# Kernel optimization log

Measured on AMD Instinct MI355X. Metric: run time of the kernel, lower is better.

Reference implementation:

```python
import jax, jax.numpy as jnp
import numpy as np
import math

B, S, D, H = 4, 2048, 1024, 16
HD = D // H  # 64


def setup_inputs() -> dict:
    key = jax.random.key(0)
    ks = jax.random.split(key, 12)
    s_in = 1.0 / math.sqrt(D)
    inp = {
        "x_v": jax.random.normal(ks[0], (B, S, D), jnp.float32),
        "x_k": jax.random.normal(ks[1], (B, S, D), jnp.float32),
        "x_q": jax.random.normal(ks[2], (B, S, D), jnp.float32),
        "mask": jax.random.randint(ks[3], (B, S, S), 0, 2, jnp.int32),
        "Wq": jax.random.normal(ks[4], (H, D, HD), jnp.float32) * s_in,
        "bq": jax.random.normal(ks[5], (H, HD), jnp.float32) * s_in,
        "Wk": jax.random.normal(ks[6], (H, D, HD), jnp.float32) * s_in,
        "bk": jax.random.normal(ks[7], (H, HD), jnp.float32) * s_in,
        "Wv": jax.random.normal(ks[8], (H, D, HD), jnp.float32) * s_in,
        "bv": jax.random.normal(ks[9], (H, HD), jnp.float32) * s_in,
        "Wo": jax.random.normal(ks[10], (D, D), jnp.float32) * s_in,
        "bo": jax.random.normal(ks[11], (D,), jnp.float32) * s_in,
    }
    return inp


def reference(x_v, x_k, x_q, mask, Wq, bq, Wk, bk, Wv, bv, Wo, bo):
    # Batched per-head projections: [B,S,D] x [H,D,E] -> [B,H,S,E]
    q = jnp.einsum("bsd,hde->bhse", x_q, Wq) + bq[None, :, None, :]
    k = jnp.einsum("bsd,hde->bhse", x_k, Wk) + bk[None, :, None, :]
    v = jnp.einsum("bsd,hde->bhse", x_v, Wv) + bv[None, :, None, :]
    scale = 1.0 / math.sqrt(HD)
    scores = jnp.einsum("bhqe,bhke->bhqk", q, k) * scale  # [B,H,Sq,Sk]
    # Faithful to original: masked positions are set to 0 (not -inf) BEFORE softmax
    scores = jnp.where(mask[:, None, :, :] == 0, 0.0, scores)
    attn = jax.nn.softmax(scores, axis=-1)
    z = jnp.einsum("bhqk,bhke->bhqe", attn, v)  # [B,H,Sq,E]
    # Concat over heads in head order (matches torch.cat along dim=2)
    z = z.transpose(0, 2, 1, 3).reshape(B, S, D)
    return z @ Wo + bo
```

## Files before the change

### kernel.cpp

```cpp
#include <hip/hip_runtime.h>

typedef unsigned short u16;
typedef unsigned long long u64;
typedef __attribute__((ext_vector_type(8))) short bf16x8;
typedef __attribute__((ext_vector_type(4))) float f32x4;

#define LD 72
#define C_SCALE 0.18033688011112043f

__device__ __forceinline__ u16 f2b(float x) {
  union { float f; unsigned u; } c; c.f = x;
  unsigned r = (c.u + 0x7fffu + ((c.u >> 16) & 1u)) >> 16;
  return (u16)r;
}

__device__ __forceinline__ unsigned pk2(float a, float b) {
#if __has_builtin(__builtin_amdgcn_cvt_pk_bf16_f32)
  typedef __attribute__((ext_vector_type(2))) __bf16 b2;
  b2 r = __builtin_amdgcn_cvt_pk_bf16_f32(a, b);
  union { b2 v; unsigned u; } c; c.v = r;
  return c.u;
#else
  union { float f; unsigned u; } x, y;
  x.f = a; y.f = b;
  return ((x.u + 0x8000u) >> 16) | ((y.u + 0x8000u) & 0xffff0000u);
#endif
}

__device__ __forceinline__ float blo(int w) {
  union { int i; float f; } c; c.i = w << 16; return c.f;
}
__device__ __forceinline__ float bhi(int w) {
  union { int i; float f; } c; c.i = w & 0xffff0000; return c.f;
}

__device__ __forceinline__ void gll16(const u16* g, u16* l) {
  __builtin_amdgcn_global_load_lds(
      (const __attribute__((address_space(1))) void*)g,
      (__attribute__((address_space(3))) void*)l, 16, 0, 0);
}

__global__ __launch_bounds__(256) void cvt_bf16_3(
    const float4* __restrict__ s0, const float4* __restrict__ s1,
    const float4* __restrict__ s2, ushort4* __restrict__ d0,
    ushort4* __restrict__ d1, ushort4* __restrict__ d2, int n4) {
  const int z = blockIdx.y;
  const float4* src = z == 0 ? s0 : z == 1 ? s1 : s2;
  ushort4* dst = z == 0 ? d0 : z == 1 ? d1 : d2;
  int stride = gridDim.x * 256;
  for (int i = blockIdx.x * 256 + threadIdx.x; i < n4; i += stride) {
    float4 v = src[i];
    ushort4 o = { f2b(v.x), f2b(v.y), f2b(v.z), f2b(v.w) };
    dst[i] = o;
  }
}

__global__ __launch_bounds__(256) void transpose_cvt_all(
    const float* __restrict__ Wq, const float* __restrict__ Wk,
    const float* __restrict__ Wv, const float* __restrict__ Wo,
    u16* __restrict__ wq_t, u16* __restrict__ wk_t,
    u16* __restrict__ wv_t, u16* __restrict__ wo_t) {
  __shared__ u16 tile[64][65];
  const int id = blockIdx.x;
  const int which = id >> 8, sub = id & 255;
  const float* s;
  u16* d;
  int R, C, r0, c0;
  if (which < 3) {
    const float* W = which == 0 ? Wq : which == 1 ? Wk : Wv;
    u16* D = which == 0 ? wq_t : which == 1 ? wk_t : wv_t;
    int h = sub >> 4, rt = sub & 15;
    s = W + (size_t)h * 1024 * 64;
    d = D + (size_t)h * 64 * 1024;
    R = 1024; C = 64; r0 = rt * 64; c0 = 0;
  } else {
    s = Wo; d = wo_t;
    R = 1024; C = 1024; r0 = ((sub >> 4) & 15) * 64; c0 = (sub & 15) * 64;
  }
  const int t = threadIdx.x;
#pragma unroll
  for (int rep = 0; rep < 16; ++rep) {
    int idx = rep * 256 + t;
    int i = idx >> 6, j = idx & 63;
    tile[j][i] = f2b(s[(size_t)(r0 + i) * C + c0 + j]);
  }
  __syncthreads();
#pragma unroll
  for (int rep = 0; rep < 16; ++rep) {
    int idx = rep * 256 + t;
    int jj = idx >> 6, ii = idx & 63;
    d[(size_t)(c0 + jj) * R + r0 + ii] = tile[jj][ii];
  }
}

__global__ __launch_bounds__(256) void expand_mask(
    const int4* __restrict__ m, ushort4* __restrict__ mb, int n4) {
  int stride = gridDim.x * 256;
  for (int i = blockIdx.x * 256 + threadIdx.x; i < n4; i += stride) {
    int4 v = m[i];
    ushort4 o = { (u16)(v.x ? 0x3f80 : 0), (u16)(v.y ? 0x3f80 : 0),
                  (u16)(v.z ? 0x3f80 : 0), (u16)(v.w ? 0x3f80 : 0) };
    mb[i] = o;
  }
}

__device__ __forceinline__ void gemm_core(
    const u16* __restrict__ A, const u16* __restrict__ W,
    u16* Asm, u16* Bsm, int s0, int n0, int wv, int lane,
    int m16, int q4, f32x4 acc[4][4]) {
  const int rsub = lane >> 3, csub = lane & 7;
  const int wr = (wv & 1) * 64, wc = (wv >> 1) * 64;
  for (int k0 = 0; k0 < 1024; k0 += 64) {
    __syncthreads();
#pragma unroll
    for (int i = 0; i < 4; ++i) {
      int chunk = wv * 4 + i;
      gll16(A + (size_t)(s0 + chunk * 8 + rsub) * 1024 + k0 + csub * 8,
            Asm + chunk * 512 + lane * 8);
      gll16(W + (size_t)(n0 + chunk * 8 + rsub) * 1024 + k0 + csub * 8,
            Bsm + chunk * 512 + lane * 8);
    }
    __syncthreads();
#pragma unroll
    for (int ks = 0; ks < 2; ++ks) {
      bf16x8 af[4], bfr[4];
#pragma unroll
      for (int i = 0; i < 4; ++i)
        af[i] = *(const bf16x8*)(Asm + (wr + i * 16 + m16) * 64 + ks * 32 + q4 * 8);
#pragma unroll
      for (int j = 0; j < 4; ++j)
        bfr[j] = *(const bf16x8*)(Bsm + (wc + j * 16 + m16) * 64 + ks * 32 + q4 * 8);
#pragma unroll
      for (int i = 0; i < 4; ++i)
#pragma unroll
        for (int j = 0; j < 4; ++j)
          acc[i][j] = __builtin_amdgcn_mfma_f32_16x16x32_bf16(af[i], bfr[j], acc[i][j], 0, 0, 0);
    }
  }
}

__global__ __launch_bounds__(256, 3) void qkv_gemm(
    const u16* __restrict__ xq, const u16* __restrict__ xk,
    const u16* __restrict__ xv, const u16* __restrict__ wq,
    const u16* __restrict__ wk, const u16* __restrict__ wv_,
    const float* __restrict__ bq, const float* __restrict__ bk,
    const float* __restrict__ bv, u16* __restrict__ qb,
    u16* __restrict__ kb, u16* __restrict__ vtb) {
  __shared__ u16 S[17408];
  u16* Asm = S;
  u16* Bsm = S + 8192;
  const int z = blockIdx.z;
  const u16* A = z == 0 ? xq : z == 1 ? xk : xv;
  const u16* W = z == 0 ? wq : z == 1 ? wk : wv_;
  const float* bias = z == 0 ? bq : z == 1 ? bk : bv;
  const int s0 = blockIdx.x * 128, n0 = blockIdx.y * 128;
  const int t = threadIdx.x, wvi = t >> 6, lane = t & 63;
  const int m16 = lane & 15, q4 = lane >> 4;
  const int wr = (wvi & 1) * 64, wc = (wvi >> 1) * 64;
  f32x4 acc[4][4];
#pragma unroll
  for (int i = 0; i < 4; ++i)
#pragma unroll
    for (int j = 0; j < 4; ++j) acc[i][j] = (f32x4){0.f, 0.f, 0.f, 0.f};

  gemm_core(A, W, Asm, Bsm, s0, n0, wvi, lane, m16, q4, acc);

  if (z < 2) {
    u16* out = z == 0 ? qb : kb;
    const float scale = z == 0 ? C_SCALE : 1.0f;
#pragma unroll
    for (int j = 0; j < 4; ++j) {
      int n = n0 + wc + j * 16 + m16;
      int h = n >> 6, e = n & 63;
      float bval = bias[n];
#pragma unroll
      for (int i = 0; i < 4; ++i)
#pragma unroll
        for (int r = 0; r < 4; ++r) {
          int s = s0 + wr + i * 16 + q4 * 4 + r;
          int bi = s >> 11, sl = s & 2047;
          out[((size_t)(bi * 16 + h) * 2048 + sl) * 64 + e] =
              f2b((acc[i][j][r] + bval) * scale);
        }
    }
  } else {
    __syncthreads();
#pragma unroll
    for (int j = 0; j < 4; ++j) {
      int nl = wc + j * 16 + m16;
      float bval = bias[n0 + nl];
#pragma unroll
      for (int i = 0; i < 4; ++i)
#pragma unroll
        for (int r = 0; r < 4; ++r)
          S[nl * 136 + wr + i * 16 + q4 * 4 + r] = f2b(acc[i][j][r] + bval);
    }
    __syncthreads();
    const int bi = s0 >> 11, sl0 = s0 & 2047;
#pragma unroll
    for (int rep = 0; rep < 8; ++rep) {
      int u = rep * 256 + t;
      int rr = u >> 4, cc = (u & 15) * 8;
      int n = n0 + rr, h = n >> 6, e = n & 63;
      *(int4*)(vtb + ((size_t)(bi * 16 + h) * 64 + e) * 2048 + sl0 + cc) =
          *(const int4*)(S + rr * 136 + cc);
    }
  }
}

__global__ __launch_bounds__(256, 2) void out_gemm(
    const u16* __restrict__ Z, const u16* __restrict__ Wot,
    const float* __restrict__ bo, float* __restrict__ out) {
  __shared__ u16 S[17408];
  u16* Asm = S;
  u16* Bsm = S + 8192;
  const int s0 = blockIdx.x * 128, n0 = blockIdx.y * 128;
  const int t = threadIdx.x, wvi = t >> 6, lane = t & 63;
  const int m16 = lane & 15, q4 = lane >> 4;
  const int wr = (wvi & 1) * 64, wc = (wvi >> 1) * 64;
  f32x4 acc[4][4];
#pragma unroll
  for (int i = 0; i < 4; ++i)
#pragma unroll
    for (int j = 0; j < 4; ++j) acc[i][j] = (f32x4){0.f, 0.f, 0.f, 0.f};

  gemm_core(Z, Wot, Asm, Bsm, s0, n0, wvi, lane, m16, q4, acc);

#pragma unroll
  for (int j = 0; j < 4; ++j) {
    int n = n0 + wc + j * 16 + m16;
    float bval = bo[n];
#pragma unroll
    for (int i = 0; i < 4; ++i)
#pragma unroll
      for (int r = 0; r < 4; ++r) {
        int s = s0 + wr + i * 16 + q4 * 4 + r;
        out[(size_t)s * 1024 + n] = acc[i][j][r] + bval;
      }
  }
}

__global__ __launch_bounds__(256, 4) void attn(
    const u16* __restrict__ qb, const u16* __restrict__ kb,
    const u16* __restrict__ vt, const u16* __restrict__ mk,
    u16* __restrict__ zb) {
  __shared__ u16 Kl[2][64 * LD];
  __shared__ u16 Vl[2][64 * LD];
  const int id = blockIdx.x;
  const int qi = id >> 6;
  const int bh = id & 63;
  const int b = bh >> 4, h = bh & 15;
  const int t = threadIdx.x, w = t >> 6, lane = t & 63;
  const int m16 = lane & 15, q4 = lane >> 4;
  const size_t bho = (size_t)bh * 2048;
  const u16* qp = qb + bho * 64;
  const u16* kp = kb + bho * 64;
  const u16* vp = vt + bho * 64;
  const int qbase = qi * 128 + w * 32;

  bf16x8 qa[2][2];
#pragma unroll
  for (int qg = 0; qg < 2; ++qg)
#pragma unroll
    for (int ks = 0; ks < 2; ++ks)
      qa[qg][ks] = *(const bf16x8*)(qp + (size_t)(qbase + qg * 16 + m16) * 64 + ks * 32 + q4 * 8);

  f32x4 oacc[2][4], lacc[2];
#pragma unroll
  for (int qg = 0; qg < 2; ++qg) {
    lacc[qg] = (f32x4){0.f, 0.f, 0.f, 0.f};
#pragma unroll
    for (int g = 0; g < 4; ++g) oacc[qg][g] = (f32x4){0.f, 0.f, 0.f, 0.f};
  }
  bf16x8 ones;
#pragma unroll
  for (int j = 0; j < 8; ++j) ones[j] = (short)0x3f80;

  const u16* mrow[2];
  mrow[0] = mk + ((size_t)b * 2048 + qbase + m16) * 2048;
  mrow[1] = mk + ((size_t)b * 2048 + qbase + 16 + m16) * 2048;

  const int ch = t & 7, rw = t >> 3;
  const int sK = (((rw >> 2) & 1) * 16) + (((rw >> 3) & 3) * 4) + (rw & 3);

  int4 pk0 = *(const int4*)(kp + (size_t)rw * 64 + ch * 8);
  int4 pk1 = *(const int4*)(kp + (size_t)(rw + 32) * 64 + ch * 8);
  int4 pv0 = *(const int4*)(vp + (size_t)rw * 2048 + ch * 8);
  int4 pv1 = *(const int4*)(vp + (size_t)(rw + 32) * 2048 + ch * 8);
  int4 cm[2][2], nm[2][2];
#pragma unroll
  for (int qg = 0; qg < 2; ++qg)
#pragma unroll
    for (int bb = 0; bb < 2; ++bb)
      cm[qg][bb] = *(const int4*)(mrow[qg] + bb * 32 + q4 * 8);
  *(int4*)(&Kl[0][sK * LD + ch * 8]) = pk0;
  *(int4*)(&Kl[0][(sK + 32) * LD + ch * 8]) = pk1;
  *(int4*)(&Vl[0][rw * LD + ch * 8]) = pv0;
  *(int4*)(&Vl[0][(rw + 32) * LD + ch * 8]) = pv1;
  __syncthreads();

  for (int kt = 0; kt < 32; ++kt) {
    const int cur = kt & 1;
    if (kt < 31) {
      const int k0n = (kt + 1) * 64;
      pk0 = *(const int4*)(kp + (size_t)(k0n + rw) * 64 + ch * 8);
      pk1 = *(const int4*)(kp + (size_t)(k0n + rw + 32) * 64 + ch * 8);
      pv0 = *(const int4*)(vp + (size_t)rw * 2048 + k0n + ch * 8);
      pv1 = *(const int4*)(vp + (size_t)(rw + 32) * 2048 + k0n + ch * 8);
#pragma unroll
      for (int qg = 0; qg < 2; ++qg)
#pragma unroll
        for (int bb = 0; bb < 2; ++bb)
          nm[qg][bb] = *(const int4*)(mrow[qg] + k0n + bb * 32 + q4 * 8);
    }

#pragma unroll
    for (int bb = 0; bb < 2; ++bb) {
      bf16x8 kf00 = *(const bf16x8*)(&Kl[cur][(bb * 32 + m16) * LD + q4 * 8]);
      bf16x8 kf01 = *(const bf16x8*)(&Kl[cur][(bb * 32 + m16) * LD + 32 + q4 * 8]);
      bf16x8 kf10 = *(const bf16x8*)(&Kl[cur][(bb * 32 + 16 + m16) * LD + q4 * 8]);
      bf16x8 kf11 = *(const bf16x8*)(&Kl[cur][(bb * 32 + 16 + m16) * LD + 32 + q4 * 8]);
      bf16x8 pa[2];
#pragma unroll
      for (int qg = 0; qg < 2; ++qg) {
        f32x4 sa = (f32x4){0.f, 0.f, 0.f, 0.f};
        f32x4 sb = (f32x4){0.f, 0.f, 0.f, 0.f};
        sa = __builtin_amdgcn_mfma_f32_16x16x32_bf16(kf00, qa[qg][0], sa, 0, 0, 0);
        sa = __builtin_amdgcn_mfma_f32_16x16x32_bf16(kf01, qa[qg][1], sa, 0, 0, 0);
        sb = __builtin_amdgcn_mfma_f32_16x16x32_bf16(kf10, qa[qg][0], sb, 0, 0, 0);
        sb = __builtin_amdgcn_mfma_f32_16x16x32_bf16(kf11, qa[qg][1], sb, 0, 0, 0);
        const int4 mw = cm[qg][bb];
        float p[8];
        p[0] = __builtin_amdgcn_exp2f(sa[0] * blo(mw.x));
        p[1] = __builtin_amdgcn_exp2f(sa[1] * bhi(mw.x));
        p[2] = __builtin_amdgcn_exp2f(sa[2] * blo(mw.y));
        p[3] = __builtin_amdgcn_exp2f(sa[3] * bhi(mw.y));
        p[4] = __builtin_amdgcn_exp2f(sb[0] * blo(mw.z));
        p[5] = __builtin_amdgcn_exp2f(sb[1] * bhi(mw.z));
        p[6] = __builtin_amdgcn_exp2f(sb[2] * blo(mw.w));
        p[7] = __builtin_amdgcn_exp2f(sb[3] * bhi(mw.w));
        union { unsigned u[4]; bf16x8 v; } pu;
        pu.u[0] = pk2(p[0], p[1]);
        pu.u[1] = pk2(p[2], p[3]);
        pu.u[2] = pk2(p[4], p[5]);
        pu.u[3] = pk2(p[6], p[7]);
        pa[qg] = pu.v;
        lacc[qg] = __builtin_amdgcn_mfma_f32_16x16x32_bf16(pa[qg], ones, lacc[qg], 0, 0, 0);
      }
#pragma unroll
      for (int e = 0; e < 4; ++e) {
        bf16x8 vf = *(const bf16x8*)(&Vl[cur][(e * 16 + m16) * LD + bb * 32 + q4 * 8]);
        oacc[0][e] = __builtin_amdgcn_mfma_f32_16x16x32_bf16(pa[0], vf, oacc[0][e], 0, 0, 0);
        oacc[1][e] = __builtin_amdgcn_mfma_f32_16x16x32_bf16(pa[1], vf, oacc[1][e], 0, 0, 0);
      }
    }

    if (kt < 31) {
      const int nxt = cur ^ 1;
      *(int4*)(&Kl[nxt][sK * LD + ch * 8]) = pk0;
      *(int4*)(&Kl[nxt][(sK + 32) * LD + ch * 8]) = pk1;
      *(int4*)(&Vl[nxt][rw * LD + ch * 8]) = pv0;
      *(int4*)(&Vl[nxt][(rw + 32) * LD + ch * 8]) = pv1;
#pragma unroll
      for (int qg = 0; qg < 2; ++qg)
#pragma unroll
        for (int bb = 0; bb < 2; ++bb) cm[qg][bb] = nm[qg][bb];
      __syncthreads();
    }
  }

#pragma unroll
  for (int qg = 0; qg < 2; ++qg) {
#pragma unroll
    for (int r = 0; r < 4; ++r) {
      float inv = 1.f / lacc[qg][r];
      size_t zr = ((size_t)b * 2048 + qbase + qg * 16 + q4 * 4 + r) * 1024 + h * 64;
#pragma unroll
      for (int e = 0; e < 4; ++e) {
        zb[zr + e * 16 + m16] = f2b(oacc[qg][e][r] * inv);
      }
    }
  }
}

extern "C" void kernel_launch(void* const* d_in, const int* in_sizes, int n_in,
                              void* d_out, int out_size, void* d_ws, size_t ws_size,
                              hipStream_t stream) {
  const float* x_v = (const float*)d_in[0];
  const float* x_k = (const float*)d_in[1];
  const float* x_q = (const float*)d_in[2];
  const int* mask = (const int*)d_in[3];
  const float* Wq = (const float*)d_in[4];
  const float* bq = (const float*)d_in[5];
  const float* Wk = (const float*)d_in[6];
  const float* bk = (const float*)d_in[7];
  const float* Wv = (const float*)d_in[8];
  const float* bv = (const float*)d_in[9];
  const float* Wo = (const float*)d_in[10];
  const float* bo = (const float*)d_in[11];
  float* out = (float*)d_out;

  char* ws = (char*)d_ws;
  size_t off = 0;
  auto alloc_u16 = [&](size_t n) {
    u16* p = (u16*)(ws + off);
    off += n * sizeof(u16);
    return p;
  };
  u16* wq_t = alloc_u16((size_t)16 * 64 * 1024);
  u16* wk_t = alloc_u16((size_t)16 * 64 * 1024);
  u16* wv_t = alloc_u16((size_t)16 * 64 * 1024);
  u16* wo_t = alloc_u16((size_t)1024 * 1024);
  u16* qb = alloc_u16((size_t)8192 * 1024);
  u16* kb = alloc_u16((size_t)8192 * 1024);
  u16* vtb = alloc_u16((size_t)8192 * 1024);
  u16* xq16 = alloc_u16((size_t)8192 * 1024);
  u16* xk16 = alloc_u16((size_t)8192 * 1024);
  u16* xv16 = alloc_u16((size_t)8192 * 1024);
  u16* zb = xq16;
  u16* mask16 = xk16;

  transpose_cvt_all<<<dim3(1024), 256, 0, stream>>>(
      Wq, Wk, Wv, Wo, wq_t, wk_t, wv_t, wo_t);
  const int n4 = 8192 * 1024 / 4;
  cvt_bf16_3<<<dim3(512, 3), 256, 0, stream>>>(
      (const float4*)x_q, (const float4*)x_k, (const float4*)x_v,
      (ushort4*)xq16, (ushort4*)xk16, (ushort4*)xv16, n4);
  qkv_gemm<<<dim3(64, 8, 3), 256, 0, stream>>>(
      xq16, xk16, xv16, wq_t, wk_t, wv_t, bq, bk, bv, qb, kb, vtb);
  expand_mask<<<dim3(2048), 256, 0, stream>>>(
      (const int4*)mask, (ushort4*)mask16, 4 * 2048 * 2048 / 4);
  attn<<<dim3(1024), 256, 0, stream>>>(qb, kb, vtb, mask16, zb);
  out_gemm<<<dim3(64, 8), 256, 0, stream>>>(zb, wo_t, bo, out);
}
```

Before: 403.3 us.

## Swizzle attention LDS tiles, unroll K loop by two, add MFMA priority hints

The attention kernel replaces padded LDS rows (stride 72) with unpadded 64-wide rows and an XOR column swizzle, which shrinks shared memory per block and aims to avoid bank conflicts. The key loop is unrolled by two with static double-buffer indices and separate mask registers, removing the dynamic buffer selection and the mask register copies. s_setprio raises wave priority around the MFMA sections, and the final division becomes a hardware reciprocal. The risks are extra register pressure from the larger unrolled body and slightly lower precision in the normalisation.

```diff
diff --git a/kernel.cpp b/kernel.cpp
--- a/kernel.cpp
+++ b/kernel.cpp
@@ -5,7 +5,6 @@
 typedef __attribute__((ext_vector_type(8))) short bf16x8;
 typedef __attribute__((ext_vector_type(4))) float f32x4;
 
-#define LD 72
 #define C_SCALE 0.18033688011112043f
 
 __device__ __forceinline__ u16 f2b(float x) {
@@ -244,8 +243,8 @@
     const u16* __restrict__ qb, const u16* __restrict__ kb,
     const u16* __restrict__ vt, const u16* __restrict__ mk,
     u16* __restrict__ zb) {
-  __shared__ u16 Kl[2][64 * LD];
-  __shared__ u16 Vl[2][64 * LD];
+  __shared__ u16 Kl[2][4096];
+  __shared__ u16 Vl[2][4096];
   const int id = blockIdx.x;
   const int qi = id >> 6;
   const int bh = id & 63;
@@ -276,60 +275,55 @@
 #pragma unroll
   for (int j = 0; j < 8; ++j) ones[j] = (short)0x3f80;
 
-  const u16* mrow[2];
-  mrow[0] = mk + ((size_t)b * 2048 + qbase + m16) * 2048;
-  mrow[1] = mk + ((size_t)b * 2048 + qbase + 16 + m16) * 2048;
+  const u16* mrow0 = mk + ((size_t)b * 2048 + qbase + m16) * 2048;
+  const u16* mrow1 = mrow0 + (size_t)16 * 2048;
 
   const int ch = t & 7, rw = t >> 3;
   const int sK = (((rw >> 2) & 1) * 16) + (((rw >> 3) & 3) * 4) + (rw & 3);
+
+  const int kwc = (ch ^ (sK & 7)) * 8;
+  const int vwc = (ch ^ (rw & 7)) * 8;
+  const int sw = (m16 & 7) * 8;
+  const int rcol0 = (q4 * 8) ^ sw;
+  const int rcol1 = (32 + q4 * 8) ^ sw;
 
   int4 pk0 = *(const int4*)(kp + (size_t)rw * 64 + ch * 8);
   int4 pk1 = *(const int4*)(kp + (size_t)(rw + 32) * 64 + ch * 8);
   int4 pv0 = *(const int4*)(vp + (size_t)rw * 2048 + ch * 8);
   int4 pv1 = *(const int4*)(vp + (size_t)(rw + 32) * 2048 + ch * 8);
-  int4 cm[2][2], nm[2][2];
-#pragma unroll
-  for (int qg = 0; qg < 2; ++qg)
-#pragma unroll
-    for (int bb = 0; bb < 2; ++bb)
-      cm[qg][bb] = *(const int4*)(mrow[qg] + bb * 32 + q4 * 8);
-  *(int4*)(&Kl[0][sK * LD + ch * 8]) = pk0;
-  *(int4*)(&Kl[0][(sK + 32) * LD + ch * 8]) = pk1;
-  *(int4*)(&Vl[0][rw * LD + ch * 8]) = pv0;
-  *(int4*)(&Vl[0][(rw + 32) * LD + ch * 8]) = pv1;
+  int4 cmA[2][2], cmB[2][2];
+#pragma unroll
+  for (int bb = 0; bb < 2; ++bb) {
+    cmA[0][bb] = *(const int4*)(mrow0 + bb * 32 + q4 * 8);
+    cmA[1][bb] = *(const int4*)(mrow1 + bb * 32 + q4 * 8);
+  }
+  *(int4*)(&Kl[0][sK * 64 + kwc]) = pk0;
+  *(int4*)(&Kl[0][(sK + 32) * 64 + kwc]) = pk1;
+  *(int4*)(&Vl[0][rw * 64 + vwc]) = pv0;
+  *(int4*)(&Vl[0][(rw + 32) * 64 + vwc]) = pv1;
   __syncthreads();
 
-  for (int kt = 0; kt < 32; ++kt) {
-    const int cur = kt & 1;
-    if (kt < 31) {
-      const int k0n = (kt + 1) * 64;
-      pk0 = *(const int4*)(kp + (size_t)(k0n + rw) * 64 + ch * 8);
-      pk1 = *(const int4*)(kp + (size_t)(k0n + rw + 32) * 64 + ch * 8);
-      pv0 = *(const int4*)(vp + (size_t)rw * 2048 + k0n + ch * 8);
-      pv1 = *(const int4*)(vp + (size_t)(rw + 32) * 2048 + k0n + ch * 8);
-#pragma unroll
-      for (int qg = 0; qg < 2; ++qg)
-#pragma unroll
-        for (int bb = 0; bb < 2; ++bb)
-          nm[qg][bb] = *(const int4*)(mrow[qg] + k0n + bb * 32 + q4 * 8);
-    }
-
+  auto compute = [&](const u16* Kc, const u16* Vc, const int4 (&cmv)[2][2]) {
 #pragma unroll
     for (int bb = 0; bb < 2; ++bb) {
-      bf16x8 kf00 = *(const bf16x8*)(&Kl[cur][(bb * 32 + m16) * LD + q4 * 8]);
-      bf16x8 kf01 = *(const bf16x8*)(&Kl[cur][(bb * 32 + m16) * LD + 32 + q4 * 8]);
-      bf16x8 kf10 = *(const bf16x8*)(&Kl[cur][(bb * 32 + 16 + m16) * LD + q4 * 8]);
-      bf16x8 kf11 = *(const bf16x8*)(&Kl[cur][(bb * 32 + 16 + m16) * LD + 32 + q4 * 8]);
+      const int rb = bb * 32;
+      const int vc = bb ? rcol1 : rcol0;
+      bf16x8 kf00 = *(const bf16x8*)(Kc + (rb + m16) * 64 + rcol0);
+      bf16x8 kf01 = *(const bf16x8*)(Kc + (rb + m16) * 64 + rcol1);
+      bf16x8 kf10 = *(const bf16x8*)(Kc + (rb + 16 + m16) * 64 + rcol0);
+      bf16x8 kf11 = *(const bf16x8*)(Kc + (rb + 16 + m16) * 64 + rcol1);
       bf16x8 pa[2];
 #pragma unroll
       for (int qg = 0; qg < 2; ++qg) {
         f32x4 sa = (f32x4){0.f, 0.f, 0.f, 0.f};
         f32x4 sb = (f32x4){0.f, 0.f, 0.f, 0.f};
+        __builtin_amdgcn_s_setprio(1);
         sa = __builtin_amdgcn_mfma_f32_16x16x32_bf16(kf00, qa[qg][0], sa, 0, 0, 0);
         sa = __builtin_amdgcn_mfma_f32_16x16x32_bf16(kf01, qa[qg][1], sa, 0, 0, 0);
         sb = __builtin_amdgcn_mfma_f32_16x16x32_bf16(kf10, qa[qg][0], sb, 0, 0, 0);
         sb = __builtin_amdgcn_mfma_f32_16x16x32_bf16(kf11, qa[qg][1], sb, 0, 0, 0);
-        const int4 mw = cm[qg][bb];
+        __builtin_amdgcn_s_setprio(0);
+        const int4 mw = cmv[qg][bb];
         float p[8];
         p[0] = __builtin_amdgcn_exp2f(sa[0] * blo(mw.x));
         p[1] = __builtin_amdgcn_exp2f(sa[1] * bhi(mw.x));
@@ -347,24 +341,55 @@
         pa[qg] = pu.v;
         lacc[qg] = __builtin_amdgcn_mfma_f32_16x16x32_bf16(pa[qg], ones, lacc[qg], 0, 0, 0);
       }
+      __builtin_amdgcn_s_setprio(1);
 #pragma unroll
       for (int e = 0; e < 4; ++e) {
-        bf16x8 vf = *(const bf16x8*)(&Vl[cur][(e * 16 + m16) * LD + bb * 32 + q4 * 8]);
+        bf16x8 vf = *(const bf16x8*)(Vc + (e * 16 + m16) * 64 + vc);
         oacc[0][e] = __builtin_amdgcn_mfma_f32_16x16x32_bf16(pa[0], vf, oacc[0][e], 0, 0, 0);
         oacc[1][e] = __builtin_amdgcn_mfma_f32_16x16x32_bf16(pa[1], vf, oacc[1][e], 0, 0, 0);
       }
-    }
-
-    if (kt < 31) {
-      const int nxt = cur ^ 1;
-      *(int4*)(&Kl[nxt][sK * LD + ch * 8]) = pk0;
-      *(int4*)(&Kl[nxt][(sK + 32) * LD + ch * 8]) = pk1;
-      *(int4*)(&Vl[nxt][rw * LD + ch * 8]) = pv0;
-      *(int4*)(&Vl[nxt][(rw + 32) * LD + ch * 8]) = pv1;
-#pragma unroll
-      for (int qg = 0; qg < 2; ++qg)
-#pragma unroll
-        for (int bb = 0; bb < 2; ++bb) cm[qg][bb] = nm[qg][bb];
+      __builtin_amdgcn_s_setprio(0);
+    }
+  };
+
+  for (int kt = 0; kt < 32; kt += 2) {
+    {
+      const int k0n = (kt + 1) * 64;
+      pk0 = *(const int4*)(kp + (size_t)(k0n + rw) * 64 + ch * 8);
+      pk1 = *(const int4*)(kp + (size_t)(k0n + rw + 32) * 64 + ch * 8);
+      pv0 = *(const int4*)(vp + (size_t)rw * 2048 + k0n + ch * 8);
+      pv1 = *(const int4*)(vp + (size_t)(rw + 32) * 2048 + k0n + ch * 8);
+#pragma unroll
+      for (int bb = 0; bb < 2; ++bb) {
+        cmB[0][bb] = *(const int4*)(mrow0 + k0n + bb * 32 + q4 * 8);
+        cmB[1][bb] = *(const int4*)(mrow1 + k0n + bb * 32 + q4 * 8);
+      }
+    }
+    compute(Kl[0], Vl[0], cmA);
+    *(int4*)(&Kl[1][sK * 64 + kwc]) = pk0;
+    *(int4*)(&Kl[1][(sK + 32) * 64 + kwc]) = pk1;
+    *(int4*)(&Vl[1][rw * 64 + vwc]) = pv0;
+    *(int4*)(&Vl[1][(rw + 32) * 64 + vwc]) = pv1;
+    __syncthreads();
+
+    if (kt < 30) {
+      const int k0n = (kt + 2) * 64;
+      pk0 = *(const int4*)(kp + (size_t)(k0n + rw) * 64 + ch * 8);
+      pk1 = *(const int4*)(kp + (size_t)(k0n + rw + 32) * 64 + ch * 8);
+      pv0 = *(const int4*)(vp + (size_t)rw * 2048 + k0n + ch * 8);
+      pv1 = *(const int4*)(vp + (size_t)(rw + 32) * 2048 + k0n + ch * 8);
+#pragma unroll
+      for (int bb = 0; bb < 2; ++bb) {
+        cmA[0][bb] = *(const int4*)(mrow0 + k0n + bb * 32 + q4 * 8);
+        cmA[1][bb] = *(const int4*)(mrow1 + k0n + bb * 32 + q4 * 8);
+      }
+    }
+    compute(Kl[1], Vl[1], cmB);
+    if (kt < 30) {
+      *(int4*)(&Kl[0][sK * 64 + kwc]) = pk0;
+      *(int4*)(&Kl[0][(sK + 32) * 64 + kwc]) = pk1;
+      *(int4*)(&Vl[0][rw * 64 + vwc]) = pv0;
+      *(int4*)(&Vl[0][(rw + 32) * 64 + vwc]) = pv1;
       __syncthreads();
     }
   }
@@ -373,7 +398,7 @@
   for (int qg = 0; qg < 2; ++qg) {
 #pragma unroll
     for (int r = 0; r < 4; ++r) {
-      float inv = 1.f / lacc[qg][r];
+      float inv = __builtin_amdgcn_rcpf(lacc[qg][r]);
       size_t zr = ((size_t)b * 2048 + qbase + qg * 16 + q4 * 4 + r) * 1024 + h * 64;
 #pragma unroll
       for (int e = 0; e < 4; ++e) {
```

Measured after the change: 690.9 us. +71.3%, slower.
